# Kernel optimization log

Measured on AMD Instinct MI355X. Metric: run time of the kernel, lower is better.

The kernel has to match this reference:

```python
import jax, jax.numpy as jnp
import numpy as np

L, H, NH, V, T, B, K = 12, 768, 12, 30522, 512, 4, 21
DH = H // NH
INV_SQRT_DH = 1.0 / float(np.sqrt(DH))
NEG = -1e4  # BERT additive mask value
LN_EPS = 1e-12


def _ln(x, g, b):
    m = x.mean(-1, keepdims=True)
    v = jnp.var(x, axis=-1, keepdims=True)
    return (x - m) * jax.lax.rsqrt(v + LN_EPS) * g + b


def _encoder(input_ids, attention_mask, word_emb, pos_emb, tok_emb, emb_g, emb_b,
             Wqkv, bqkv, Wo, bo, ln1_g, ln1_b, W1, b1, W2, b2, ln2_g, ln2_b):
    Bv, Tv = input_ids.shape
    h = word_emb[input_ids] + pos_emb[None, :Tv] + tok_emb[0]  # token_type_ids = 0
    h = _ln(h, emb_g, emb_b)
    bias = (1.0 - attention_mask[:, None, None, :].astype(h.dtype)) * NEG  # [B,1,1,T]

    def layer(h, xs):
        wqkv, bq, wo, bo_, g1, b1_, w1, bb1, w2, bb2, g2, b2_ = xs
        qkv = h @ wqkv + bq  # [B,T,3H]
        q, k, v = jnp.split(qkv, 3, axis=-1)
        def hd(x):
            return x.reshape(Bv, Tv, NH, DH).transpose(0, 2, 1, 3)
        q, k, v = hd(q), hd(k), hd(v)
        scores = jnp.einsum('bhqd,bhkd->bhqk', q, k) * INV_SQRT_DH + bias
        ctx = jnp.einsum('bhqk,bhkd->bhqd', jax.nn.softmax(scores, axis=-1), v)
        ctx = ctx.transpose(0, 2, 1, 3).reshape(Bv, Tv, H)
        h = _ln(h + ctx @ wo + bo_, g1, b1_)  # post-LN (BERT)
        ff = jax.nn.gelu(h @ w1 + bb1, approximate=False) @ w2 + bb2
        h = _ln(h + ff, g2, b2_)
        return h, None

    h, _ = jax.lax.scan(layer, h, (Wqkv, bqkv, Wo, bo, ln1_g, ln1_b, W1, b1, W2, b2, ln2_g, ln2_b))
    return h


def _crf_nll(emissions, tags, mask, start, end, trans):
    # emissions [B,T,K], tags [B,T] int, mask [B,T] bool; torchcrf reduction='mean'
    Bv, Tv, Kv = emissions.shape
    maskf = mask.astype(emissions.dtype)
    # numerator: score of the gold path
    num = start[tags[:, 0]] + emissions[jnp.arange(Bv), 0, tags[:, 0]]
    em_t = jnp.take_along_axis(emissions, tags[..., None], axis=-1)[..., 0]  # [B,T]
    tr_t = trans[tags[:, :-1], tags[:, 1:]]  # [B,T-1]
    num = num + jnp.sum((tr_t + em_t[:, 1:]) * maskf[:, 1:], axis=1)
    last_idx = mask.sum(axis=1).astype(jnp.int32) - 1
    last_tag = jnp.take_along_axis(tags, last_idx[:, None], axis=1)[:, 0]
    num = num + end[last_tag]
    # denominator: forward algorithm (logsumexp recursion over time)
    alpha0 = start[None, :] + emissions[:, 0]  # [B,K]

    def step(alpha, xs):
        em, m = xs  # em [B,K], m [B] bool
        nxt = jax.scipy.special.logsumexp(alpha[:, :, None] + trans[None] + em[:, None, :], axis=1)
        return jnp.where(m[:, None], nxt, alpha), None

    alpha, _ = jax.lax.scan(step, alpha0, (emissions[:, 1:].transpose(1, 0, 2), mask[:, 1:].T))
    den = jax.scipy.special.logsumexp(alpha + end[None, :], axis=1)
    return -(num - den).mean()


def _viterbi(emissions, mask, start, end, trans):
    # Returns [B,T] int32 best paths; padded tail repeats the last valid tag.
    Bv, Tv, Kv = emissions.shape
    score0 = start[None, :] + emissions[:, 0]
    ident = jnp.broadcast_to(jnp.arange(Kv), (Bv, Kv))

    def step(score, xs):
        em, m = xs
        cand = score[:, :, None] + trans[None]  # [B,K_prev,K_next]
        idx = jnp.where(m[:, None], jnp.argmax(cand, axis=1), ident)
        nxt = jnp.max(cand, axis=1) + em
        return jnp.where(m[:, None], nxt, score), idx

    score, hist = jax.lax.scan(step, score0, (emissions[:, 1:].transpose(1, 0, 2), mask[:, 1:].T))
    last = jnp.argmax(score + end[None, :], axis=1)  # [B]

    def back(nxt_tag, idx):
        prev = jnp.take_along_axis(idx, nxt_tag[:, None], axis=1)[:, 0]
        return prev, nxt_tag

    tag0, rest = jax.lax.scan(back, last, hist, reverse=True)  # rest[i] = tag at t=i+1
    return jnp.concatenate([tag0[None], rest], axis=0).T.astype(jnp.int32)


def setup_inputs():
    key = jax.random.key(0)
    ks = jax.random.split(key, 16)
    s = 0.02

    def n(k, shape):
        return (s * jax.random.normal(k, shape)).astype(jnp.float32)

    def u(k, shape):
        return jax.random.uniform(k, shape, minval=-0.1, maxval=0.1).astype(jnp.float32)

    p = {}
    p['input_ids'] = jax.random.randint(ks[0], (B, T), 0, V)
    lengths = jax.random.randint(ks[1], (B,), T // 2, T + 1)
    p['attention_mask'] = (jnp.arange(T)[None, :] < lengths[:, None]).astype(jnp.int32)
    p['valid_mask'] = p['attention_mask']
    p['labels'] = jax.random.randint(ks[2], (B, T), 0, K)
    p['word_emb'] = n(ks[3], (V, H))
    p['pos_emb'] = n(ks[4], (T, H))
    p['tok_emb'] = n(ks[5], (2, H))
    p['emb_g'] = jnp.ones((H,), jnp.float32)
    p['emb_b'] = jnp.zeros((H,), jnp.float32)
    p['Wqkv'] = n(ks[6], (L, H, 3 * H))
    p['bqkv'] = jnp.zeros((L, 3 * H), jnp.float32)
    p['Wo'] = n(ks[7], (L, H, H))
    p['bo'] = jnp.zeros((L, H), jnp.float32)
    p['ln1_g'] = jnp.ones((L, H), jnp.float32)
    p['ln1_b'] = jnp.zeros((L, H), jnp.float32)
    p['W1'] = n(ks[8], (L, H, 4 * H))
    p['b1'] = jnp.zeros((L, 4 * H), jnp.float32)
    p['W2'] = n(ks[9], (L, 4 * H, H))
    p['b2'] = jnp.zeros((L, H), jnp.float32)
    p['ln2_g'] = jnp.ones((L, H), jnp.float32)
    p['ln2_b'] = jnp.zeros((L, H), jnp.float32)
    p['Wc'] = n(ks[10], (H, K))
    p['bc'] = jnp.zeros((K,), jnp.float32)
    p['crf_start'] = u(ks[11], (K,))
    p['crf_end'] = u(ks[12], (K,))
    p['crf_trans'] = u(ks[13], (K, K))
    return p


def reference(input_ids, attention_mask, valid_mask, labels,
              word_emb, pos_emb, tok_emb, emb_g, emb_b,
              Wqkv, bqkv, Wo, bo, ln1_g, ln1_b, W1, b1, W2, b2, ln2_g, ln2_b,
              Wc, bc, crf_start, crf_end, crf_trans):
    h = _encoder(input_ids, attention_mask, word_emb, pos_emb, tok_emb, emb_g, emb_b,
                 Wqkv, bqkv, Wo, bo, ln1_g, ln1_b, W1, b1, W2, b2, ln2_g, ln2_b)
    emissions = h @ Wc + bc  # dropout is identity in eval/reference mode
    mask = attention_mask.astype(bool)
    nll = _crf_nll(emissions, labels, mask, crf_start, crf_end, crf_trans)
    decoded = _viterbi(emissions, mask, crf_start, crf_end, crf_trans)
    return nll, decoded
```

## Files before the change

### kernel.cpp

```cpp
#include <hip/hip_runtime.h>
#include <math.h>

constexpr int NLAYER = 12;
constexpr int H = 768;
constexpr int NH = 12;
constexpr int DH = 64;
constexpr int T = 512;
constexpr int B = 4;
constexpr int K = 21;
constexpr int BT = B * T;
constexpr float NEGB = -10000.0f;
constexpr float LNEPS = 1e-12f;
constexpr float INV_SQRT_DH = 0.125f;

typedef __attribute__((ext_vector_type(8))) short bf16x8;
typedef __attribute__((ext_vector_type(4))) float f32x4;

__device__ __forceinline__ float wave_sum_f(float v) {
#pragma unroll
  for (int off = 32; off > 0; off >>= 1) v += __shfl_xor(v, off);
  return v;
}
__device__ __forceinline__ int wave_sum_i(int v) {
#pragma unroll
  for (int off = 32; off > 0; off >>= 1) v += __shfl_xor(v, off);
  return v;
}

__device__ __forceinline__ unsigned short f32_bf16_rn(float x) {
  unsigned int u = __float_as_uint(x);
  u += 0x7fffu + ((u >> 16) & 1u);
  return (unsigned short)(u >> 16);
}
__device__ __forceinline__ void split_bf16(float x, unsigned short& h, unsigned short& l) {
  h = f32_bf16_rn(x);
  float hf = __uint_as_float((unsigned int)h << 16);
  l = f32_bf16_rn(x - hf);
}

__device__ __forceinline__ void block_reduce_sum2(float& s, float& q) {
  __shared__ float red[8];
  s = wave_sum_f(s);
  q = wave_sum_f(q);
  int lane = threadIdx.x & 63, wid = threadIdx.x >> 6;
  if (lane == 0) { red[wid] = s; red[4 + wid] = q; }
  __syncthreads();
  s = red[0] + red[1] + red[2] + red[3];
  q = red[4] + red[5] + red[6] + red[7];
}

__global__ __launch_bounds__(256) void embed_ln_kernel(
    const int* __restrict__ ids, const float* __restrict__ wemb,
    const float* __restrict__ pemb, const float* __restrict__ temb,
    const float* __restrict__ g, const float* __restrict__ bta,
    float* __restrict__ h) {
  int row = blockIdx.x;
  int t = row % T;
  int id = ids[row];
  const float* wp = wemb + (size_t)id * H;
  const float* pp = pemb + (size_t)t * H;
  float x[3];
  float s = 0.f, q = 0.f;
#pragma unroll
  for (int i = 0; i < 3; i++) {
    int c = threadIdx.x + i * 256;
    x[i] = wp[c] + pp[c] + temb[c];
    s += x[i];
    q += x[i] * x[i];
  }
  block_reduce_sum2(s, q);
  float mean = s * (1.0f / H);
  float var = q * (1.0f / H) - mean * mean;
  float inv = rsqrtf(var + LNEPS);
#pragma unroll
  for (int i = 0; i < 3; i++) {
    int c = threadIdx.x + i * 256;
    h[(size_t)row * H + c] = (x[i] - mean) * inv * g[c] + bta[c];
  }
}

__global__ __launch_bounds__(256) void add_ln_kernel(
    float* __restrict__ h, const float* __restrict__ add,
    const float* __restrict__ g, const float* __restrict__ bta) {
  int row = blockIdx.x;
  size_t base = (size_t)row * H;
  float x[3];
  float s = 0.f, q = 0.f;
#pragma unroll
  for (int i = 0; i < 3; i++) {
    int c = threadIdx.x + i * 256;
    x[i] = h[base + c] + add[base + c];
    s += x[i];
    q += x[i] * x[i];
  }
  block_reduce_sum2(s, q);
  float mean = s * (1.0f / H);
  float var = q * (1.0f / H) - mean * mean;
  float inv = rsqrtf(var + LNEPS);
#pragma unroll
  for (int i = 0; i < 3; i++) {
    int c = threadIdx.x + i * 256;
    h[base + c] = (x[i] - mean) * inv * g[c] + bta[c];
  }
}

template <int BM, int BN, bool GELU>
__global__ __launch_bounds__(256) void gemm_mfma_kernel(
    const float* __restrict__ A, const float* __restrict__ W,
    const float* __restrict__ bias, float* __restrict__ C, int N, int Kd) {
  constexpr int WTM = BM / 2, WTN = BN / 2;
  constexpr int FM = WTM / 16, FN = WTN / 16;
  constexpr int STRIDE = 40;
  __shared__ short Ah[BM * STRIDE];
  __shared__ short Al[BM * STRIDE];
  __shared__ short Wh[BN * STRIDE];
  __shared__ short Wl[BN * STRIDE];
  int tid = threadIdx.x;
  int lane = tid & 63, wid = tid >> 6;
  int wr = wid >> 1, wc = wid & 1;
  int bm = blockIdx.y * BM, bn = blockIdx.x * BN;
  f32x4 acc[FM][FN] = {};

  for (int k0 = 0; k0 < Kd; k0 += 32) {
    alignas(16) unsigned short ahb[16], alb[16], whb[16], wlb[16];
    int am, ak, wn, wk;
    if constexpr (BM == 128) {
      am = tid >> 1; ak = (tid & 1) * 16;
      const float* ap = A + (size_t)(bm + am) * Kd + k0 + ak;
      float av[16];
      *(float4*)&av[0]  = *(const float4*)(ap + 0);
      *(float4*)&av[4]  = *(const float4*)(ap + 4);
      *(float4*)&av[8]  = *(const float4*)(ap + 8);
      *(float4*)&av[12] = *(const float4*)(ap + 12);
#pragma unroll
      for (int q = 0; q < 16; q++) split_bf16(av[q], ahb[q], alb[q]);
      wn = tid & 127; wk = (tid >> 7) * 16;
      const float* wp = W + (size_t)(k0 + wk) * N + bn + wn;
#pragma unroll
      for (int q = 0; q < 16; q++) {
        float wv = wp[(size_t)q * N];
        split_bf16(wv, whb[q], wlb[q]);
      }
    } else {
      am = tid >> 2; ak = (tid & 3) * 8;
      const float* ap = A + (size_t)(bm + am) * Kd + k0 + ak;
      float av[8];
      *(float4*)&av[0] = *(const float4*)(ap + 0);
      *(float4*)&av[4] = *(const float4*)(ap + 4);
#pragma unroll
      for (int q = 0; q < 8; q++) split_bf16(av[q], ahb[q], alb[q]);
      wn = tid & 63; wk = (tid >> 6) * 8;
      const float* wp = W + (size_t)(k0 + wk) * N + bn + wn;
#pragma unroll
      for (int q = 0; q < 8; q++) {
        float wv = wp[(size_t)q * N];
        split_bf16(wv, whb[q], wlb[q]);
      }
    }
    __syncthreads();
    if constexpr (BM == 128) {
      *(uint4*)&Ah[am * STRIDE + ak]     = *(uint4*)&ahb[0];
      *(uint4*)&Ah[am * STRIDE + ak + 8] = *(uint4*)&ahb[8];
      *(uint4*)&Al[am * STRIDE + ak]     = *(uint4*)&alb[0];
      *(uint4*)&Al[am * STRIDE + ak + 8] = *(uint4*)&alb[8];
      *(uint4*)&Wh[wn * STRIDE + wk]     = *(uint4*)&whb[0];
      *(uint4*)&Wh[wn * STRIDE + wk + 8] = *(uint4*)&whb[8];
      *(uint4*)&Wl[wn * STRIDE + wk]     = *(uint4*)&wlb[0];
      *(uint4*)&Wl[wn * STRIDE + wk + 8] = *(uint4*)&wlb[8];
    } else {
      *(uint4*)&Ah[am * STRIDE + ak] = *(uint4*)&ahb[0];
      *(uint4*)&Al[am * STRIDE + ak] = *(uint4*)&alb[0];
      *(uint4*)&Wh[wn * STRIDE + wk] = *(uint4*)&whb[0];
      *(uint4*)&Wl[wn * STRIDE + wk] = *(uint4*)&wlb[0];
    }
    __syncthreads();
    bf16x8 af_h[FM], af_l[FM], wf_h[FN], wf_l[FN];
    int lr = lane & 15, lg = lane >> 4;
#pragma unroll
    for (int i = 0; i < FM; i++) {
      int e = (wr * WTM + i * 16 + lr) * STRIDE + lg * 8;
      af_h[i] = *(const bf16x8*)&Ah[e];
      af_l[i] = *(const bf16x8*)&Al[e];
    }
#pragma unroll
    for (int j = 0; j < FN; j++) {
      int e = (wc * WTN + j * 16 + lr) * STRIDE + lg * 8;
      wf_h[j] = *(const bf16x8*)&Wh[e];
      wf_l[j] = *(const bf16x8*)&Wl[e];
    }
#pragma unroll
    for (int i = 0; i < FM; i++)
#pragma unroll
      for (int j = 0; j < FN; j++) {
        acc[i][j] = __builtin_amdgcn_mfma_f32_16x16x32_bf16(af_h[i], wf_h[j], acc[i][j], 0, 0, 0);
        acc[i][j] = __builtin_amdgcn_mfma_f32_16x16x32_bf16(af_l[i], wf_h[j], acc[i][j], 0, 0, 0);
        acc[i][j] = __builtin_amdgcn_mfma_f32_16x16x32_bf16(af_h[i], wf_l[j], acc[i][j], 0, 0, 0);
      }
  }
  int lr = lane & 15, lg = lane >> 4;
#pragma unroll
  for (int i = 0; i < FM; i++) {
#pragma unroll
    for (int j = 0; j < FN; j++) {
      int row = bm + wr * WTM + i * 16 + lg * 4;
      int col = bn + wc * WTN + j * 16 + lr;
      float bv = bias[col];
#pragma unroll
      for (int r = 0; r < 4; r++) {
        float v = acc[i][j][r] + bv;
        if (GELU) v = 0.5f * v * (1.0f + erff(v * 0.70710678118654752f));
        C[(size_t)(row + r) * N + col] = v;
      }
    }
  }
}

__global__ __launch_bounds__(256) void qk_kernel(
    const float* __restrict__ qkv, const int* __restrict__ mask,
    float* __restrict__ S) {
  int bh = blockIdx.z;
  int b = bh / NH, hh = bh % NH;
  int i0 = blockIdx.y * 64, j0 = blockIdx.x * 64;
  __shared__ float Qs[64][64];
  __shared__ float Ks[64][64];
  int tid = threadIdx.x;
  int r = tid >> 2;
  int cseg = (tid & 3) * 16;
  const float* qbase = qkv + (size_t)(b * T + i0 + r) * (3 * H) + hh * DH;
  const float* kbase = qkv + (size_t)(b * T + j0 + r) * (3 * H) + H + hh * DH;
#pragma unroll
  for (int ss = 0; ss < 4; ss++) {
    int c = cseg + ss * 4;
    float4 qa = *(const float4*)(qbase + c);
    float4 ka = *(const float4*)(kbase + c);
    Qs[c + 0][r] = qa.x; Qs[c + 1][r] = qa.y; Qs[c + 2][r] = qa.z; Qs[c + 3][r] = qa.w;
    Ks[c + 0][r] = ka.x; Ks[c + 1][r] = ka.y; Ks[c + 2][r] = ka.z; Ks[c + 3][r] = ka.w;
  }
  __syncthreads();
  int tx = tid & 15, ty = tid >> 4;
  float acc[4][4] = {};
#pragma unroll 4
  for (int d = 0; d < 64; d++) {
    float a_[4], b_[4];
    *(float4*)a_ = *(const float4*)&Qs[d][ty * 4];
    *(float4*)b_ = *(const float4*)&Ks[d][tx * 4];
#pragma unroll
    for (int i = 0; i < 4; i++)
#pragma unroll
      for (int j = 0; j < 4; j++)
        acc[i][j] = fmaf(a_[i], b_[j], acc[i][j]);
  }
  float bj[4];
#pragma unroll
  for (int q = 0; q < 4; q++)
    bj[q] = (1.0f - (float)mask[b * T + j0 + tx * 4 + q]) * NEGB;
#pragma unroll
  for (int i = 0; i < 4; i++) {
    int gi = i0 + ty * 4 + i;
    int gj = j0 + tx * 4;
    float4 o;
    o.x = acc[i][0] * INV_SQRT_DH + bj[0];
    o.y = acc[i][1] * INV_SQRT_DH + bj[1];
    o.z = acc[i][2] * INV_SQRT_DH + bj[2];
    o.w = acc[i][3] * INV_SQRT_DH + bj[3];
    *(float4*)(S + ((size_t)bh * T + gi) * T + gj) = o;
  }
}

__global__ __launch_bounds__(128) void softmax_kernel(float* __restrict__ S) {
  size_t row = blockIdx.x;
  float* p = S + row * T;
  int tid = threadIdx.x;
  float4 v = *(float4*)(p + tid * 4);
  float m = fmaxf(fmaxf(v.x, v.y), fmaxf(v.z, v.w));
#pragma unroll
  for (int off = 32; off > 0; off >>= 1) m = fmaxf(m, __shfl_xor(m, off));
  __shared__ float redm[2];
  __shared__ float reds[2];
  int wid = tid >> 6;
  if ((tid & 63) == 0) redm[wid] = m;
  __syncthreads();
  m = fmaxf(redm[0], redm[1]);
  v.x = __expf(v.x - m);
  v.y = __expf(v.y - m);
  v.z = __expf(v.z - m);
  v.w = __expf(v.w - m);
  float s = v.x + v.y + v.z + v.w;
  s = wave_sum_f(s);
  if ((tid & 63) == 0) reds[wid] = s;
  __syncthreads();
  s = reds[0] + reds[1];
  float inv = 1.0f / s;
  v.x *= inv; v.y *= inv; v.z *= inv; v.w *= inv;
  *(float4*)(p + tid * 4) = v;
}

__global__ __launch_bounds__(256) void pv_kernel(
    const float* __restrict__ S, const float* __restrict__ qkv,
    float* __restrict__ ctx) {
  int bh = blockIdx.y;
  int b = bh / NH, hh = bh % NH;
  int i0 = blockIdx.x * 64;
  __shared__ float Ps[64][68];
  __shared__ float Vs[64][64];
  int tid = threadIdx.x;
  int r = tid >> 2;
  int cseg = (tid & 3) * 16;
  int tx = tid & 15, ty = tid >> 4;
  float acc[4][4] = {};
  const float* srow = S + ((size_t)bh * T + i0 + r) * T;
  const float* vbase = qkv + (size_t)(b * T) * (3 * H) + 2 * H + hh * DH;
  for (int k0 = 0; k0 < T; k0 += 64) {
    __syncthreads();
#pragma unroll
    for (int ss = 0; ss < 4; ss++) {
      int c = cseg + ss * 4;
      *(float4*)&Ps[r][c] = *(const float4*)(srow + k0 + c);
      *(float4*)&Vs[r][c] = *(const float4*)(vbase + (size_t)(k0 + r) * (3 * H) + c);
    }
    __syncthreads();
#pragma unroll
    for (int kk = 0; kk < 64; kk += 4) {
      float p_[4][4], v_[4][4];
#pragma unroll
      for (int i = 0; i < 4; i++)
        *(float4*)p_[i] = *(const float4*)&Ps[ty * 4 + i][kk];
#pragma unroll
      for (int s = 0; s < 4; s++)
        *(float4*)v_[s] = *(const float4*)&Vs[kk + s][tx * 4];
#pragma unroll
      for (int i = 0; i < 4; i++)
#pragma unroll
        for (int s = 0; s < 4; s++)
#pragma unroll
          for (int j = 0; j < 4; j++)
            acc[i][j] = fmaf(p_[i][s], v_[s][j], acc[i][j]);
    }
  }
#pragma unroll
  for (int i = 0; i < 4; i++) {
    int gi = i0 + ty * 4 + i;
    float* cp = ctx + (size_t)(b * T + gi) * H + hh * DH + tx * 4;
    float4 o;
    o.x = acc[i][0]; o.y = acc[i][1]; o.z = acc[i][2]; o.w = acc[i][3];
    *(float4*)cp = o;
  }
}

__global__ __launch_bounds__(256) void classifier_kernel(
    const float* __restrict__ h, const float* __restrict__ Wc,
    const float* __restrict__ bc, float* __restrict__ em) {
  int id = blockIdx.x * 256 + threadIdx.x;
  if (id >= BT * K) return;
  int row = id / K, k = id % K;
  float acc = bc[k];
  const float* hr = h + (size_t)row * H;
  for (int d = 0; d < H; d++) acc = fmaf(hr[d], Wc[d * K + k], acc);
  em[id] = acc;
}

__global__ __launch_bounds__(64) void crf_fused_kernel(
    const float* __restrict__ em, const int* __restrict__ labels,
    const int* __restrict__ mask, const float* __restrict__ start,
    const float* __restrict__ endv, const float* __restrict__ trans,
    float* __restrict__ parts, float* __restrict__ outdec) {
  __shared__ float em_s[T * K];
  __shared__ int mask_s[T];
  __shared__ unsigned char hist_s[(T - 1) * K];
  __shared__ float sc_s[32];
  int b = blockIdx.x & 3;
  int role = blockIdx.x >> 2;
  int j = threadIdx.x;
  const float* eb = em + (size_t)b * T * K;
  for (int i = j; i < T * K / 4; i += 64)
    ((float4*)em_s)[i] = ((const float4*)eb)[i];
  for (int i = j; i < T; i += 64) mask_s[i] = mask[b * T + i];
  __syncthreads();
  bool act = (j < K);
  float tr[K];
  if (act) {
#pragma unroll
    for (int i = 0; i < K; i++) tr[i] = trans[i * K + j];
  } else {
#pragma unroll
    for (int i = 0; i < K; i++) tr[i] = 0.f;
  }

  if (role == 0) {
    const int* tb = labels + b * T;
    float numloc = 0.f;
    int cnt = 0;
    for (int t = j; t < T; t += 64) {
      cnt += mask_s[t];
      if (t >= 1 && mask_s[t]) {
        int tp = tb[t - 1], tc = tb[t];
        numloc += trans[tp * K + tc] + em_s[t * K + tc];
      }
    }
    float num = wave_sum_f(numloc);
    int cnttot = wave_sum_i(cnt);
    float alpha = -3.0e38f;
    if (act) alpha = start[j] + em_s[j];
    for (int t = 1; t < T; t++) {
      if (mask_s[t]) {
        float vals[K];
        float m = -3.0e38f;
#pragma unroll
        for (int i = 0; i < K; i++) {
          float v = __shfl(alpha, i) + tr[i];
          vals[i] = v;
          m = fmaxf(m, v);
        }
        float ssum = 0.f;
#pragma unroll
        for (int i = 0; i < K; i++) ssum += __expf(vals[i] - m);
        float emv = act ? em_s[t * K + j] : 0.f;
        float nxt = __logf(ssum) + m + emv;
        if (act) alpha = nxt;
      }
    }
    float aj = act ? (alpha + endv[j]) : -3.0e38f;
    float mm = aj;
#pragma unroll
    for (int off = 32; off > 0; off >>= 1) mm = fmaxf(mm, __shfl_xor(mm, off));
    float e = act ? __expf(aj - mm) : 0.f;
    float s = wave_sum_f(e);
    float den = __logf(s) + mm;
    if (j == 0) {
      int tag0 = tb[0];
      int lastidx = cnttot - 1;
      float numtot = num + start[tag0] + em_s[tag0] + endv[tb[lastidx]];
      parts[b] = numtot - den;
    }
  } else {
    float score = -3.0e38f;
    if (act) score = start[j] + em_s[j];
    for (int t = 1; t < T; t++) {
      int m = mask_s[t];
      float best = -3.0e38f;
      int bi = 0;
#pragma unroll
      for (int i = 0; i < K; i++) {
        float v = __shfl(score, i) + tr[i];
        if (v > best) { best = v; bi = i; }
      }
      if (act) {
        hist_s[(t - 1) * K + j] = (unsigned char)(m ? bi : j);
        if (m) score = best + em_s[t * K + j];
      }
    }
    if (act) sc_s[j] = score + endv[j];
    __syncthreads();
    if (j == 0) {
      float best = -3.0e38f;
      int cur = 0;
#pragma unroll
      for (int i = 0; i < K; i++)
        if (sc_s[i] > best) { best = sc_s[i]; cur = i; }
      outdec[b * T + (T - 1)] = (float)cur;
      for (int t = T - 1; t >= 1; t--) {
        cur = hist_s[(t - 1) * K + cur];
        outdec[b * T + (t - 1)] = (float)cur;
      }
    }
  }
}

__global__ void nll_final_kernel(const float* __restrict__ parts,
                                 float* __restrict__ out) {
  out[0] = -0.25f * (parts[0] + parts[1] + parts[2] + parts[3]);
}

extern "C" void kernel_launch(void* const* d_in, const int* in_sizes, int n_in,
                              void* d_out, int out_size, void* d_ws, size_t ws_size,
                              hipStream_t stream) {
  (void)in_sizes; (void)n_in; (void)out_size; (void)ws_size;
  const int* ids    = (const int*)d_in[0];
  const int* amask  = (const int*)d_in[1];
  const int* labels = (const int*)d_in[3];
  const float* wemb = (const float*)d_in[4];
  const float* pemb = (const float*)d_in[5];
  const float* temb = (const float*)d_in[6];
  const float* eg   = (const float*)d_in[7];
  const float* ebta = (const float*)d_in[8];
  const float* Wqkv = (const float*)d_in[9];
  const float* bqkv = (const float*)d_in[10];
  const float* Wo   = (const float*)d_in[11];
  const float* bo   = (const float*)d_in[12];
  const float* ln1g = (const float*)d_in[13];
  const float* ln1b = (const float*)d_in[14];
  const float* W1   = (const float*)d_in[15];
  const float* b1   = (const float*)d_in[16];
  const float* W2   = (const float*)d_in[17];
  const float* b2   = (const float*)d_in[18];
  const float* ln2g = (const float*)d_in[19];
  const float* ln2b = (const float*)d_in[20];
  const float* Wc   = (const float*)d_in[21];
  const float* bc   = (const float*)d_in[22];
  const float* cst  = (const float*)d_in[23];
  const float* cen  = (const float*)d_in[24];
  const float* ctr  = (const float*)d_in[25];
  float* out = (float*)d_out;

  float* ws   = (float*)d_ws;
  float* h    = ws;
  float* qkv  = h + (size_t)BT * H;
  float* ctx  = qkv + (size_t)BT * 3 * H;
  float* tmp  = ctx + (size_t)BT * H;
  float* big  = tmp + (size_t)BT * H;
  float* em   = big + (size_t)B * NH * T * T;
  float* parts = em + (size_t)BT * K;

  embed_ln_kernel<<<BT, 256, 0, stream>>>(ids, wemb, pemb, temb, eg, ebta, h);

  for (int l = 0; l < NLAYER; l++) {
    const float* wqkv_l = Wqkv + (size_t)l * H * 3 * H;
    const float* bqkv_l = bqkv + (size_t)l * 3 * H;
    const float* wo_l   = Wo + (size_t)l * H * H;
    const float* bo_l   = bo + (size_t)l * H;
    const float* w1_l   = W1 + (size_t)l * H * 4 * H;
    const float* b1_l   = b1 + (size_t)l * 4 * H;
    const float* w2_l   = W2 + (size_t)l * 4 * H * H;
    const float* b2_l   = b2 + (size_t)l * H;

    gemm_mfma_kernel<128, 128, false><<<dim3(3 * H / 128, BT / 128), 256, 0, stream>>>(
        h, wqkv_l, bqkv_l, qkv, 3 * H, H);
    qk_kernel<<<dim3(T / 64, T / 64, B * NH), 256, 0, stream>>>(qkv, amask, big);
    softmax_kernel<<<B * NH * T, 128, 0, stream>>>(big);
    pv_kernel<<<dim3(T / 64, B * NH), 256, 0, stream>>>(big, qkv, ctx);
    gemm_mfma_kernel<64, 64, false><<<dim3(H / 64, BT / 64), 256, 0, stream>>>(
        ctx, wo_l, bo_l, tmp, H, H);
    add_ln_kernel<<<BT, 256, 0, stream>>>(h, tmp, ln1g + (size_t)l * H, ln1b + (size_t)l * H);
    gemm_mfma_kernel<128, 128, true><<<dim3(4 * H / 128, BT / 128), 256, 0, stream>>>(
        h, w1_l, b1_l, big, 4 * H, H);
    gemm_mfma_kernel<64, 64, false><<<dim3(H / 64, BT / 64), 256, 0, stream>>>(
        big, w2_l, b2_l, tmp, H, 4 * H);
    add_ln_kernel<<<BT, 256, 0, stream>>>(h, tmp, ln2g + (size_t)l * H, ln2b + (size_t)l * H);
  }

  classifier_kernel<<<(BT * K + 255) / 256, 256, 0, stream>>>(h, Wc, bc, em);
  crf_fused_kernel<<<8, 64, 0, stream>>>(em, labels, amask, cst, cen, ctr, parts, out + 1);
  nll_final_kernel<<<1, 1, 0, stream>>>(parts, out);
}
```

Before: 3.935 ms.

## Pre-split operands to bf16 hi/lo and use direct-to-LDS GEMM loads

The GEMMs no longer convert fp32 to bf16 hi/lo inside the main loop. Each layer's weights are transposed and split once by a conversion kernel, and activations are split by the LayerNorm, PV and new fsplit kernels. A new 128x128 GEMM then streams the pre-split tiles straight into LDS with global_load_lds. The CRF forward and Viterbi recursions also switch from shuffles to readlane, with tree reductions and a multiply-by-exp(trans) form. This trades per-tile conversion work and strided weight loads for extra conversion kernels, more workspace, and a single-buffered load/compute loop.

```diff
diff --git a/kernel.cpp b/kernel.cpp
--- a/kernel.cpp
+++ b/kernel.cpp
@@ -15,6 +15,7 @@
 
 typedef __attribute__((ext_vector_type(8))) short bf16x8;
 typedef __attribute__((ext_vector_type(4))) float f32x4;
+typedef __attribute__((ext_vector_type(4))) unsigned short u16x4;
 
 __device__ __forceinline__ float wave_sum_f(float v) {
 #pragma unroll
@@ -26,7 +27,9 @@
   for (int off = 32; off > 0; off >>= 1) v += __shfl_xor(v, off);
   return v;
 }
-
+__device__ __forceinline__ float readlane_f(float v, int i) {
+  return __uint_as_float(__builtin_amdgcn_readlane(__float_as_uint(v), i));
+}
 __device__ __forceinline__ unsigned short f32_bf16_rn(float x) {
   unsigned int u = __float_as_uint(x);
   u += 0x7fffu + ((u >> 16) & 1u);
@@ -37,7 +40,6 @@
   float hf = __uint_as_float((unsigned int)h << 16);
   l = f32_bf16_rn(x - hf);
 }
-
 __device__ __forceinline__ void block_reduce_sum2(float& s, float& q) {
   __shared__ float red[8];
   s = wave_sum_f(s);
@@ -53,7 +55,8 @@
     const int* __restrict__ ids, const float* __restrict__ wemb,
     const float* __restrict__ pemb, const float* __restrict__ temb,
     const float* __restrict__ g, const float* __restrict__ bta,
-    float* __restrict__ h) {
+    float* __restrict__ h, unsigned short* __restrict__ hh,
+    unsigned short* __restrict__ hl) {
   int row = blockIdx.x;
   int t = row % T;
   int id = ids[row];
@@ -75,13 +78,19 @@
 #pragma unroll
   for (int i = 0; i < 3; i++) {
     int c = threadIdx.x + i * 256;
-    h[(size_t)row * H + c] = (x[i] - mean) * inv * g[c] + bta[c];
+    float y = (x[i] - mean) * inv * g[c] + bta[c];
+    h[(size_t)row * H + c] = y;
+    unsigned short yh, yl;
+    split_bf16(y, yh, yl);
+    hh[(size_t)row * H + c] = yh;
+    hl[(size_t)row * H + c] = yl;
   }
 }
 
 __global__ __launch_bounds__(256) void add_ln_kernel(
     float* __restrict__ h, const float* __restrict__ add,
-    const float* __restrict__ g, const float* __restrict__ bta) {
+    const float* __restrict__ g, const float* __restrict__ bta,
+    unsigned short* __restrict__ hh, unsigned short* __restrict__ hl) {
   int row = blockIdx.x;
   size_t base = (size_t)row * H;
   float x[3];
@@ -100,110 +109,129 @@
 #pragma unroll
   for (int i = 0; i < 3; i++) {
     int c = threadIdx.x + i * 256;
-    h[base + c] = (x[i] - mean) * inv * g[c] + bta[c];
-  }
-}
-
-template <int BM, int BN, bool GELU>
-__global__ __launch_bounds__(256) void gemm_mfma_kernel(
-    const float* __restrict__ A, const float* __restrict__ W,
+    float y = (x[i] - mean) * inv * g[c] + bta[c];
+    h[base + c] = y;
+    unsigned short yh, yl;
+    split_bf16(y, yh, yl);
+    hh[base + c] = yh;
+    hl[base + c] = yl;
+  }
+}
+
+__global__ __launch_bounds__(256) void wconv_kernel(
+    const float* __restrict__ w0, const float* __restrict__ w1,
+    const float* __restrict__ w2, const float* __restrict__ w3,
+    unsigned short* __restrict__ Wth, unsigned short* __restrict__ Wtl) {
+  __shared__ float tile[32][33];
+  int bid = blockIdx.x;
+  const float* src;
+  int Kd, N, tk, tn;
+  size_t off;
+  if (bid < 1728) {
+    src = w0; Kd = 768; N = 2304; tk = bid / 72; tn = bid % 72; off = 0;
+  } else if (bid < 2304) {
+    int t2 = bid - 1728; src = w1; Kd = 768; N = 768; tk = t2 / 24; tn = t2 % 24;
+    off = 1769472;
+  } else if (bid < 4608) {
+    int t2 = bid - 2304; src = w2; Kd = 768; N = 3072; tk = t2 / 96; tn = t2 % 96;
+    off = 2359296;
+  } else {
+    int t2 = bid - 4608; src = w3; Kd = 3072; N = 768; tk = t2 / 24; tn = t2 % 24;
+    off = 4718592;
+  }
+  int tid = threadIdx.x;
+  int k0 = tk * 32, n0 = tn * 32;
+  int r = tid >> 3, c = (tid & 7) * 4;
+  float4 v = *(const float4*)(src + (size_t)(k0 + r) * N + n0 + c);
+  tile[r][c + 0] = v.x; tile[r][c + 1] = v.y; tile[r][c + 2] = v.z; tile[r][c + 3] = v.w;
+  __syncthreads();
+  u16x4 hv, lv;
+#pragma unroll
+  for (int q2 = 0; q2 < 4; q2++) {
+    unsigned short sh, sl;
+    split_bf16(tile[c + q2][r], sh, sl);
+    hv[q2] = sh; lv[q2] = sl;
+  }
+  size_t dst = off + (size_t)(n0 + r) * Kd + k0 + c;
+  *(u16x4*)(Wth + dst) = hv;
+  *(u16x4*)(Wtl + dst) = lv;
+}
+
+__global__ __launch_bounds__(256) void fsplit_kernel(
+    const float* __restrict__ x, unsigned short* __restrict__ xh,
+    unsigned short* __restrict__ xl, int n4) {
+  int i = blockIdx.x * 256 + threadIdx.x;
+  if (i >= n4) return;
+  float4 v = ((const float4*)x)[i];
+  u16x4 hv, lv;
+  unsigned short sh, sl;
+  split_bf16(v.x, sh, sl); hv[0] = sh; lv[0] = sl;
+  split_bf16(v.y, sh, sl); hv[1] = sh; lv[1] = sl;
+  split_bf16(v.z, sh, sl); hv[2] = sh; lv[2] = sl;
+  split_bf16(v.w, sh, sl); hv[3] = sh; lv[3] = sl;
+  ((u16x4*)xh)[i] = hv;
+  ((u16x4*)xl)[i] = lv;
+}
+
+template <bool GELU>
+__global__ __launch_bounds__(256) void gemm_bf3_kernel(
+    const unsigned short* __restrict__ Ah, const unsigned short* __restrict__ Al,
+    const unsigned short* __restrict__ Wth, const unsigned short* __restrict__ Wtl,
     const float* __restrict__ bias, float* __restrict__ C, int N, int Kd) {
-  constexpr int WTM = BM / 2, WTN = BN / 2;
-  constexpr int FM = WTM / 16, FN = WTN / 16;
-  constexpr int STRIDE = 40;
-  __shared__ short Ah[BM * STRIDE];
-  __shared__ short Al[BM * STRIDE];
-  __shared__ short Wh[BN * STRIDE];
-  __shared__ short Wl[BN * STRIDE];
+  __shared__ short lds_s[4 * 4096];
   int tid = threadIdx.x;
   int lane = tid & 63, wid = tid >> 6;
   int wr = wid >> 1, wc = wid & 1;
-  int bm = blockIdx.y * BM, bn = blockIdx.x * BN;
-  f32x4 acc[FM][FN] = {};
+  int bm = blockIdx.y * 128, bn = blockIdx.x * 128;
+  f32x4 acc[4][4] = {};
+
+  const unsigned short* bases[4] = {Ah, Al, Wth, Wtl};
+  const unsigned short* base = bases[wid];
+  int rowbase = (wid >= 2) ? bn : bm;
+  int lrow = lane >> 2, lslot = lane & 3;
 
   for (int k0 = 0; k0 < Kd; k0 += 32) {
-    alignas(16) unsigned short ahb[16], alb[16], whb[16], wlb[16];
-    int am, ak, wn, wk;
-    if constexpr (BM == 128) {
-      am = tid >> 1; ak = (tid & 1) * 16;
-      const float* ap = A + (size_t)(bm + am) * Kd + k0 + ak;
-      float av[16];
-      *(float4*)&av[0]  = *(const float4*)(ap + 0);
-      *(float4*)&av[4]  = *(const float4*)(ap + 4);
-      *(float4*)&av[8]  = *(const float4*)(ap + 8);
-      *(float4*)&av[12] = *(const float4*)(ap + 12);
-#pragma unroll
-      for (int q = 0; q < 16; q++) split_bf16(av[q], ahb[q], alb[q]);
-      wn = tid & 127; wk = (tid >> 7) * 16;
-      const float* wp = W + (size_t)(k0 + wk) * N + bn + wn;
-#pragma unroll
-      for (int q = 0; q < 16; q++) {
-        float wv = wp[(size_t)q * N];
-        split_bf16(wv, whb[q], wlb[q]);
-      }
-    } else {
-      am = tid >> 2; ak = (tid & 3) * 8;
-      const float* ap = A + (size_t)(bm + am) * Kd + k0 + ak;
-      float av[8];
-      *(float4*)&av[0] = *(const float4*)(ap + 0);
-      *(float4*)&av[4] = *(const float4*)(ap + 4);
-#pragma unroll
-      for (int q = 0; q < 8; q++) split_bf16(av[q], ahb[q], alb[q]);
-      wn = tid & 63; wk = (tid >> 6) * 8;
-      const float* wp = W + (size_t)(k0 + wk) * N + bn + wn;
-#pragma unroll
-      for (int q = 0; q < 8; q++) {
-        float wv = wp[(size_t)q * N];
-        split_bf16(wv, whb[q], wlb[q]);
-      }
+#pragma unroll
+    for (int c = 0; c < 8; c++) {
+      int row = c * 16 + lrow;
+      const unsigned short* src = base + (size_t)(rowbase + row) * Kd + k0 + lslot * 8;
+      char* dst = ((char*)lds_s) + wid * 8192 + c * 1024 + lane * 16;
+      __builtin_amdgcn_global_load_lds(
+          (const __attribute__((address_space(1))) void*)src,
+          (__attribute__((address_space(3))) void*)dst, 16, 0, 0);
     }
     __syncthreads();
-    if constexpr (BM == 128) {
-      *(uint4*)&Ah[am * STRIDE + ak]     = *(uint4*)&ahb[0];
-      *(uint4*)&Ah[am * STRIDE + ak + 8] = *(uint4*)&ahb[8];
-      *(uint4*)&Al[am * STRIDE + ak]     = *(uint4*)&alb[0];
-      *(uint4*)&Al[am * STRIDE + ak + 8] = *(uint4*)&alb[8];
-      *(uint4*)&Wh[wn * STRIDE + wk]     = *(uint4*)&whb[0];
-      *(uint4*)&Wh[wn * STRIDE + wk + 8] = *(uint4*)&whb[8];
-      *(uint4*)&Wl[wn * STRIDE + wk]     = *(uint4*)&wlb[0];
-      *(uint4*)&Wl[wn * STRIDE + wk + 8] = *(uint4*)&wlb[8];
-    } else {
-      *(uint4*)&Ah[am * STRIDE + ak] = *(uint4*)&ahb[0];
-      *(uint4*)&Al[am * STRIDE + ak] = *(uint4*)&alb[0];
-      *(uint4*)&Wh[wn * STRIDE + wk] = *(uint4*)&whb[0];
-      *(uint4*)&Wl[wn * STRIDE + wk] = *(uint4*)&wlb[0];
-    }
-    __syncthreads();
-    bf16x8 af_h[FM], af_l[FM], wf_h[FN], wf_l[FN];
     int lr = lane & 15, lg = lane >> 4;
-#pragma unroll
-    for (int i = 0; i < FM; i++) {
-      int e = (wr * WTM + i * 16 + lr) * STRIDE + lg * 8;
-      af_h[i] = *(const bf16x8*)&Ah[e];
-      af_l[i] = *(const bf16x8*)&Al[e];
-    }
-#pragma unroll
-    for (int j = 0; j < FN; j++) {
-      int e = (wc * WTN + j * 16 + lr) * STRIDE + lg * 8;
-      wf_h[j] = *(const bf16x8*)&Wh[e];
-      wf_l[j] = *(const bf16x8*)&Wl[e];
-    }
-#pragma unroll
-    for (int i = 0; i < FM; i++)
-#pragma unroll
-      for (int j = 0; j < FN; j++) {
+    bf16x8 af_h[4], af_l[4], wf_h[4], wf_l[4];
+#pragma unroll
+    for (int i = 0; i < 4; i++) {
+      int e = (wr * 64 + i * 16 + lr) * 32 + lg * 8;
+      af_h[i] = *(const bf16x8*)&lds_s[e];
+      af_l[i] = *(const bf16x8*)&lds_s[4096 + e];
+    }
+#pragma unroll
+    for (int j = 0; j < 4; j++) {
+      int e = (wc * 64 + j * 16 + lr) * 32 + lg * 8;
+      wf_h[j] = *(const bf16x8*)&lds_s[8192 + e];
+      wf_l[j] = *(const bf16x8*)&lds_s[12288 + e];
+    }
+#pragma unroll
+    for (int i = 0; i < 4; i++)
+#pragma unroll
+      for (int j = 0; j < 4; j++) {
         acc[i][j] = __builtin_amdgcn_mfma_f32_16x16x32_bf16(af_h[i], wf_h[j], acc[i][j], 0, 0, 0);
         acc[i][j] = __builtin_amdgcn_mfma_f32_16x16x32_bf16(af_l[i], wf_h[j], acc[i][j], 0, 0, 0);
         acc[i][j] = __builtin_amdgcn_mfma_f32_16x16x32_bf16(af_h[i], wf_l[j], acc[i][j], 0, 0, 0);
       }
+    __syncthreads();
   }
   int lr = lane & 15, lg = lane >> 4;
 #pragma unroll
-  for (int i = 0; i < FM; i++) {
-#pragma unroll
-    for (int j = 0; j < FN; j++) {
-      int row = bm + wr * WTM + i * 16 + lg * 4;
-      int col = bn + wc * WTN + j * 16 + lr;
+  for (int i = 0; i < 4; i++) {
+#pragma unroll
+    for (int j = 0; j < 4; j++) {
+      int row = bm + wr * 64 + i * 16 + lg * 4;
+      int col = bn + wc * 64 + j * 16 + lr;
       float bv = bias[col];
 #pragma unroll
       for (int r = 0; r < 4; r++) {
@@ -297,7 +325,7 @@
 
 __global__ __launch_bounds__(256) void pv_kernel(
     const float* __restrict__ S, const float* __restrict__ qkv,
-    float* __restrict__ ctx) {
+    unsigned short* __restrict__ cth, unsigned short* __restrict__ ctl) {
   int bh = blockIdx.y;
   int b = bh / NH, hh = bh % NH;
   int i0 = blockIdx.x * 64;
@@ -340,10 +368,16 @@
 #pragma unroll
   for (int i = 0; i < 4; i++) {
     int gi = i0 + ty * 4 + i;
-    float* cp = ctx + (size_t)(b * T + gi) * H + hh * DH + tx * 4;
-    float4 o;
-    o.x = acc[i][0]; o.y = acc[i][1]; o.z = acc[i][2]; o.w = acc[i][3];
-    *(float4*)cp = o;
+    size_t idx = (size_t)(b * T + gi) * H + hh * DH + tx * 4;
+    u16x4 hv, lv;
+#pragma unroll
+    for (int j = 0; j < 4; j++) {
+      unsigned short sh, sl;
+      split_bf16(acc[i][j], sh, sl);
+      hv[j] = sh; lv[j] = sl;
+    }
+    *(u16x4*)(cth + idx) = hv;
+    *(u16x4*)(ctl + idx) = lv;
   }
 }
 
@@ -378,13 +412,8 @@
   __syncthreads();
   bool act = (j < K);
   float tr[K];
-  if (act) {
-#pragma unroll
-    for (int i = 0; i < K; i++) tr[i] = trans[i * K + j];
-  } else {
-#pragma unroll
-    for (int i = 0; i < K; i++) tr[i] = 0.f;
-  }
+#pragma unroll
+  for (int i = 0; i < K; i++) tr[i] = act ? trans[i * K + j] : 0.f;
 
   if (role == 0) {
     const int* tb = labels + b * T;
@@ -399,33 +428,32 @@
     }
     float num = wave_sum_f(numloc);
     int cnttot = wave_sum_i(cnt);
-    float alpha = -3.0e38f;
-    if (act) alpha = start[j] + em_s[j];
+    float etr[K];
+#pragma unroll
+    for (int i = 0; i < K; i++) etr[i] = __expf(tr[i]);
+    float alpha = act ? (start[j] + em_s[j]) : 0.f;
     for (int t = 1; t < T; t++) {
-      if (mask_s[t]) {
-        float vals[K];
-        float m = -3.0e38f;
-#pragma unroll
-        for (int i = 0; i < K; i++) {
-          float v = __shfl(alpha, i) + tr[i];
-          vals[i] = v;
-          m = fmaxf(m, v);
-        }
-        float ssum = 0.f;
-#pragma unroll
-        for (int i = 0; i < K; i++) ssum += __expf(vals[i] - m);
-        float emv = act ? em_s[t * K + j] : 0.f;
-        float nxt = __logf(ssum) + m + emv;
-        if (act) alpha = nxt;
+      if (!mask_s[t]) continue;
+      float m0 = readlane_f(alpha, 0);
+      float e = __expf(alpha - m0);
+      float p[K];
+#pragma unroll
+      for (int i = 0; i < K; i++) p[i] = readlane_f(e, i) * etr[i];
+#pragma unroll
+      for (int s = 1; s < K; s <<= 1) {
+#pragma unroll
+        for (int i = 0; i + s < K; i += 2 * s) p[i] += p[i + s];
       }
+      float nxt = __logf(p[0]) + m0 + (act ? em_s[t * K + j] : 0.f);
+      if (act) alpha = nxt;
     }
     float aj = act ? (alpha + endv[j]) : -3.0e38f;
     float mm = aj;
 #pragma unroll
     for (int off = 32; off > 0; off >>= 1) mm = fmaxf(mm, __shfl_xor(mm, off));
-    float e = act ? __expf(aj - mm) : 0.f;
-    float s = wave_sum_f(e);
-    float den = __logf(s) + mm;
+    float e2 = act ? __expf(aj - mm) : 0.f;
+    float s2 = wave_sum_f(e2);
+    float den = __logf(s2) + mm;
     if (j == 0) {
       int tag0 = tb[0];
       int lastidx = cnttot - 1;
@@ -433,20 +461,32 @@
       parts[b] = numtot - den;
     }
   } else {
-    float score = -3.0e38f;
-    if (act) score = start[j] + em_s[j];
+    float score = act ? (start[j] + em_s[j]) : 0.f;
     for (int t = 1; t < T; t++) {
       int m = mask_s[t];
-      float best = -3.0e38f;
-      int bi = 0;
-#pragma unroll
-      for (int i = 0; i < K; i++) {
-        float v = __shfl(score, i) + tr[i];
-        if (v > best) { best = v; bi = i; }
-      }
-      if (act) {
-        hist_s[(t - 1) * K + j] = (unsigned char)(m ? bi : j);
-        if (m) score = best + em_s[t * K + j];
+      if (m) {
+        float cv[K];
+        int ci[K];
+#pragma unroll
+        for (int i = 0; i < K; i++) {
+          cv[i] = readlane_f(score, i) + tr[i];
+          ci[i] = i;
+        }
+#pragma unroll
+        for (int s = 1; s < K; s <<= 1) {
+#pragma unroll
+          for (int i = 0; i + s < K; i += 2 * s) {
+            bool take = cv[i + s] > cv[i];
+            cv[i] = take ? cv[i + s] : cv[i];
+            ci[i] = take ? ci[i + s] : ci[i];
+          }
+        }
+        if (act) {
+          hist_s[(t - 1) * K + j] = (unsigned char)ci[0];
+          score = cv[0] + em_s[t * K + j];
+        }
+      } else if (act) {
+        hist_s[(t - 1) * K + j] = (unsigned char)j;
       }
     }
     if (act) sc_s[j] = score + endv[j];
@@ -502,16 +542,23 @@
   const float* ctr  = (const float*)d_in[25];
   float* out = (float*)d_out;
 
-  float* ws   = (float*)d_ws;
+  float* ws = (float*)d_ws;
   float* h    = ws;
-  float* qkv  = h + (size_t)BT * H;
-  float* ctx  = qkv + (size_t)BT * 3 * H;
-  float* tmp  = ctx + (size_t)BT * H;
-  float* big  = tmp + (size_t)BT * H;
-  float* em   = big + (size_t)B * NH * T * T;
-  float* parts = em + (size_t)BT * K;
-
-  embed_ln_kernel<<<BT, 256, 0, stream>>>(ids, wemb, pemb, temb, eg, ebta, h);
+  unsigned short* hh = (unsigned short*)(h + 1572864);
+  unsigned short* hl = (unsigned short*)(h + 1572864 + 786432);
+  float* qkv  = h + 1572864 + 786432 * 2;
+  unsigned short* cth = (unsigned short*)(qkv + 4718592);
+  unsigned short* ctl = (unsigned short*)(qkv + 4718592 + 786432);
+  float* tmp  = qkv + 4718592 + 786432 * 2;
+  float* big  = tmp + 1572864;
+  unsigned short* gh = (unsigned short*)(big + 12582912);
+  unsigned short* gl = (unsigned short*)(big + 12582912 + 3145728);
+  unsigned short* Wth = (unsigned short*)(big + 12582912 + 3145728 * 2);
+  unsigned short* Wtl = (unsigned short*)(big + 12582912 + 3145728 * 2 + 3538944);
+  float* em   = big + 12582912 + 3145728 * 2 + 3538944 * 2;
+  float* parts = em + 43008;
+
+  embed_ln_kernel<<<BT, 256, 0, stream>>>(ids, wemb, pemb, temb, eg, ebta, h, hh, hl);
 
   for (int l = 0; l < NLAYER; l++) {
     const float* wqkv_l = Wqkv + (size_t)l * H * 3 * H;
@@ -523,19 +570,22 @@
     const float* w2_l   = W2 + (size_t)l * 4 * H * H;
     const float* b2_l   = b2 + (size_t)l * H;
 
-    gemm_mfma_kernel<128, 128, false><<<dim3(3 * H / 128, BT / 128), 256, 0, stream>>>(
-        h, wqkv_l, bqkv_l, qkv, 3 * H, H);
+    wconv_kernel<<<6912, 256, 0, stream>>>(wqkv_l, wo_l, w1_l, w2_l, Wth, Wtl);
+
+    gemm_bf3_kernel<false><<<dim3(18, 16), 256, 0, stream>>>(
+        hh, hl, Wth, Wtl, bqkv_l, qkv, 3 * H, H);
     qk_kernel<<<dim3(T / 64, T / 64, B * NH), 256, 0, stream>>>(qkv, amask, big);
     softmax_kernel<<<B * NH * T, 128, 0, stream>>>(big);
-    pv_kernel<<<dim3(T / 64, B * NH), 256, 0, stream>>>(big, qkv, ctx);
-    gemm_mfma_kernel<64, 64, false><<<dim3(H / 64, BT / 64), 256, 0, stream>>>(
-        ctx, wo_l, bo_l, tmp, H, H);
-    add_ln_kernel<<<BT, 256, 0, stream>>>(h, tmp, ln1g + (size_t)l * H, ln1b + (size_t)l * H);
-    gemm_mfma_kernel<128, 128, true><<<dim3(4 * H / 128, BT / 128), 256, 0, stream>>>(
-        h, w1_l, b1_l, big, 4 * H, H);
-    gemm_mfma_kernel<64, 64, false><<<dim3(H / 64, BT / 64), 256, 0, stream>>>(
-        big, w2_l, b2_l, tmp, H, 4 * H);
-    add_ln_kernel<<<BT, 256, 0, stream>>>(h, tmp, ln2g + (size_t)l * H, ln2b + (size_t)l * H);
+    pv_kernel<<<dim3(T / 64, B * NH), 256, 0, stream>>>(big, qkv, cth, ctl);
+    gemm_bf3_kernel<false><<<dim3(6, 16), 256, 0, stream>>>(
+        cth, ctl, Wth + 1769472, Wtl + 1769472, bo_l, tmp, H, H);
+    add_ln_kernel<<<BT, 256, 0, stream>>>(h, tmp, ln1g + (size_t)l * H, ln1b + (size_t)l * H, hh, hl);
+    gemm_bf3_kernel<true><<<dim3(24, 16), 256, 0, stream>>>(
+        hh, hl, Wth + 2359296, Wtl + 2359296, b1_l, big, 4 * H, H);
+    fsplit_kernel<<<6144, 256, 0, stream>>>(big, gh, gl, 2048 * 3072 / 4);
+    gemm_bf3_kernel<false><<<dim3(6, 16), 256, 0, stream>>>(
+        gh, gl, Wth + 4718592, Wtl + 4718592, b2_l, tmp, H, 4 * H);
+    add_ln_kernel<<<BT, 256, 0, stream>>>(h, tmp, ln2g + (size_t)l * H, ln2b + (size_t)l * H, hh, hl);
   }
 
   classifier_kernel<<<(BT * K + 255) / 256, 256, 0, stream>>>(h, Wc, bc, em);
```

Measured after the change: 5.240 ms. 1.33x slower.
